# Kernel optimization log

Measured on AMD Instinct MI355X. Metric: run time of the kernel, lower is better.

## Reference

```python
import jax, jax.numpy as jnp
import numpy as np

B, S, DM, DC, L, NS = 4, 2048, 2048, 512, 4, 5  # batch, seq, d_model, d_cortical, n_layers, n_settle


def _ln(x, g, b):
    # torch nn.LayerNorm, eps=1e-5
    m = x.mean(-1, keepdims=True)
    v = ((x - m) ** 2).mean(-1, keepdims=True)
    return (x - m) * jax.lax.rsqrt(v + 1e-5) * g + b


def setup_inputs() -> dict:
    key = jax.random.key(0)
    ks = jax.random.split(key, 20)
    f = lambda k, sh: jax.random.normal(k, sh, jnp.float32) * 0.02
    return dict(
        qwen_final_hidden=jax.random.normal(ks[0], (B, S, DM), jnp.float32),
        obs=jax.random.normal(ks[1], (4, B, S, DM), jnp.float32),
        proj_W=f(ks[2], (4, DC, DM)), proj_b=f(ks[3], (4, DC)),
        fuse_W=f(ks[4], (DC, 4 * DC)), fuse_b=f(ks[5], (DC,)),
        up_W=f(ks[6], (L, DC, DC)), up_b=f(ks[7], (L, DC)),
        lateral_W=f(ks[8], (L, DC, DC)), lateral_b=f(ks[9], (L, DC)),
        precision_logit=f(ks[10], (L, DC)),
        ln_g=jnp.ones((L, DC), jnp.float32), ln_b=jnp.zeros((L, DC), jnp.float32),
        down_W=f(ks[11], (L - 1, DC, DC)), down_b=f(ks[12], (L - 1, DC)),
        out1_W=f(ks[13], (DC, DC)), out1_b=f(ks[14], (DC,)),
        out2_W=f(ks[15], (DM, DC)), out2_b=f(ks[16], (DM,)),
    )


def reference(qwen_final_hidden, obs, proj_W, proj_b, fuse_W, fuse_b,
              up_W, up_b, lateral_W, lateral_b, precision_logit,
              ln_g, ln_b, down_W, down_b, out1_W, out1_b, out2_W, out2_b):
    b, s, dm = qwen_final_hidden.shape
    # per-observed-layer input projections, concatenated along features
    proj = jnp.einsum('obsd,ocd->bsoc', obs, proj_W) + proj_b  # (B,S,4,DC)
    cat = proj.reshape(b, s, -1)
    fused = cat @ fuse_W.T + fuse_b                             # (B,S,DC)
    x0 = fused.reshape(b * s, DC)                               # per-token cortical input

    prec = jax.nn.sigmoid(precision_logit)                      # (L,DC)

    # initial bottom-up pass: activations = compress(x)
    acts = []
    x = x0
    for i in range(L):
        x = _ln(x @ up_W[i].T + up_b[i], ln_g[i], ln_b[i])
        acts.append(x)

    # settling iterations
    for _ in range(NS):
        # top-down predictions computed from pre-sweep activations
        preds = [None] * L
        for i in range(L - 1, 0, -1):
            if i < L - 1:  # top layer has no top-down weights
                preds[i - 1] = acts[i] @ down_W[i].T + down_b[i]
        x = x0
        for i in range(L):
            compressed = _ln(x @ up_W[i].T + up_b[i], ln_g[i], ln_b[i])
            target = preds[i] if preds[i] is not None else acts[i]
            werr = (compressed - target) * prec[i]
            lateral = acts[i] @ lateral_W[i].T + lateral_b[i]
            acts[i] = _ln(acts[i] + 0.5 * werr + 0.1 * lateral, ln_g[i], ln_b[i])
            x = acts[i]

    top = acts[-1]
    h = jax.nn.gelu(top @ out1_W.T + out1_b, approximate=False)
    correction = (h @ out2_W.T + out2_b).reshape(b, s, dm)
    return qwen_final_hidden + correction
```

## Files before the change

### kernel.cpp

```cpp
#include <hip/hip_runtime.h>
#include <hip/hip_bf16.h>
#include <math.h>

#define NTOK 8192
#define DMD  2048
#define DCC  512
#define TOKH 4194304

typedef __attribute__((ext_vector_type(8))) short short8;
typedef __attribute__((ext_vector_type(4))) float f32x4;

__device__ inline float bf2f(unsigned short u) {
    union { unsigned int i; float f; } x; x.i = ((unsigned int)u) << 16; return x.f;
}
__device__ inline unsigned short f2bf(float f) {
    union { float f; unsigned int i; } x; x.f = f;
    unsigned int u = x.i;
    return (unsigned short)((u + 0x7fffu + ((u >> 16) & 1u)) >> 16);
}

typedef const __attribute__((address_space(1))) unsigned int* gas1_t;
typedef __attribute__((address_space(3))) unsigned int* las3_t;
__device__ inline void async16(const void* g, void* l) {
    __builtin_amdgcn_global_load_lds(
        (gas1_t)g,
        (las3_t)(unsigned int)(unsigned long long)l, 16, 0, 0);
}

__global__ __launch_bounds__(256)
void cvt_kernel(const float* __restrict__ s, unsigned short* __restrict__ d, int n4)
{
    for (int i = blockIdx.x * 256 + threadIdx.x; i < n4; i += gridDim.x * 256) {
        float4 v = ((const float4*)s)[i];
        ushort4 o;
        o.x = f2bf(v.x); o.y = f2bf(v.y); o.z = f2bf(v.z); o.w = f2bf(v.w);
        ((ushort4*)d)[i] = o;
    }
}

struct CvtArgs { const float* src[6]; };

__global__ __launch_bounds__(256)
void wcvt_kernel(CvtArgs ca, unsigned short* __restrict__ dst)
{
    const int total = 1310720;
    for (int i = blockIdx.x * 256 + threadIdx.x; i < total; i += gridDim.x * 256) {
        const float* sp; int base;
        if      (i <  262144) { sp = ca.src[0]; base = 0;       }
        else if (i <  524288) { sp = ca.src[1]; base = 262144;  }
        else if (i <  786432) { sp = ca.src[2]; base = 524288;  }
        else if (i <  983040) { sp = ca.src[3]; base = 786432;  }
        else if (i < 1048576) { sp = ca.src[4]; base = 983040;  }
        else                  { sp = ca.src[5]; base = 1048576; }
        float4 v = ((const float4*)sp)[i - base];
        ushort4 o;
        o.x = f2bf(v.x); o.y = f2bf(v.y); o.z = f2bf(v.z); o.w = f2bf(v.w);
        ((ushort4*)dst)[i] = o;
    }
}

__global__ __launch_bounds__(256)
void ptr_kernel(const float* __restrict__ src, unsigned short* __restrict__ dst)
{
    __shared__ float t[32][33];
    const int o  = blockIdx.z;
    const int jb = blockIdx.x * 32;
    const int kb = blockIdx.y * 32;
    const int r  = threadIdx.x >> 3;
    const int c4 = (threadIdx.x & 7) * 4;
    {
        const float* s = src + ((size_t)o * DCC + kb + r) * DMD + jb + c4;
        float4 v = *(const float4*)s;
        t[r][c4+0]=v.x; t[r][c4+1]=v.y; t[r][c4+2]=v.z; t[r][c4+3]=v.w;
    }
    __syncthreads();
    {
        ushort4 u;
        u.x = f2bf(t[c4+0][r]); u.y = f2bf(t[c4+1][r]);
        u.z = f2bf(t[c4+2][r]); u.w = f2bf(t[c4+3][r]);
        *(ushort4*)(dst + ((size_t)o * DMD + jb + r) * DCC + kb + c4) = u;
    }
}

__global__ __launch_bounds__(256)
void bprime_kernel(const float* __restrict__ fuse_W, const float* __restrict__ fuse_b,
                   const float* __restrict__ proj_b, float* __restrict__ bp)
{
    const int row = blockIdx.x * 8 + (threadIdx.x >> 5);
    const int l32 = threadIdx.x & 31;
    const float* r = fuse_W + (size_t)row * (4 * DCC) + l32 * 64;
    const float* p = proj_b + l32 * 64;
    float s = 0.f;
    #pragma unroll
    for (int k = 0; k < 64; k += 4) {
        float4 v = *(const float4*)(r + k);
        float4 q = *(const float4*)(p + k);
        s += v.x*q.x + v.y*q.y + v.z*q.z + v.w*q.w;
    }
    #pragma unroll
    for (int off = 16; off; off >>= 1) s += __shfl_xor(s, off, 64);
    if (l32 == 0) bp[row] = s + fuse_b[row];
}

struct GArgs {
    const unsigned short* A[6];
    const unsigned short* W[6];
    const float*          bias[6];
    const float*          add[6];
    void*                 C[6];
};

template<bool OUTF32, bool GELU>
__global__ __launch_bounds__(256)
void gemm16(GArgs ga, int lda, int ldw, int ldadd, int ldc, int K)
{
    __shared__ unsigned short As[128 * 32];
    __shared__ unsigned short Bs[128 * 32];

    const int z    = blockIdx.z;
    const int tid  = threadIdx.x;
    const int wave = tid >> 6;
    const int lane = tid & 63;

    const int nwg   = gridDim.x * gridDim.y;
    const int bid   = blockIdx.y * gridDim.x + blockIdx.x;
    const int swz   = (bid & 7) * (nwg >> 3) + (bid >> 3);
    const int bn    = (swz % gridDim.x) * 128;
    const int bm    = (swz / gridDim.x) * 128;

    const int wr   = wave >> 1;
    const int wc   = wave & 1;

    const unsigned short* Ap = ga.A[z];
    const unsigned short* Wp = ga.W[z];

    const int lrow = lane >> 2;
    const int lcol = (lane & 3) * 8;

    f32x4 acc[4][4] = {};

    for (int k0 = 0; k0 < K; k0 += 32) {
        #pragma unroll
        for (int r = 0; r < 2; ++r) {
            int c = wave + r * 4;
            async16(Ap + (size_t)(bm + c * 16 + lrow) * lda + k0 + lcol, As + c * 512);
            async16(Wp + (size_t)(bn + c * 16 + lrow) * ldw + k0 + lcol, Bs + c * 512);
        }
        __syncthreads();

        short8 af[4], bfr[4];
        #pragma unroll
        for (int i = 0; i < 4; ++i) {
            af[i]  = *(const short8*)&As[(wr * 64 + i * 16 + (lane & 15)) * 32 + (lane >> 4) * 8];
            bfr[i] = *(const short8*)&Bs[(wc * 64 + i * 16 + (lane & 15)) * 32 + (lane >> 4) * 8];
        }
        #pragma unroll
        for (int mi = 0; mi < 4; ++mi)
            #pragma unroll
            for (int ni = 0; ni < 4; ++ni)
                acc[mi][ni] = __builtin_amdgcn_mfma_f32_16x16x32_bf16(
                    af[mi], bfr[ni], acc[mi][ni], 0, 0, 0);
        __syncthreads();
    }

    const float* bias = ga.bias[z];
    const float* add  = ga.add[z];
    #pragma unroll
    for (int ni = 0; ni < 4; ++ni) {
        int col = bn + wc * 64 + ni * 16 + (lane & 15);
        float bv = bias ? bias[col] : 0.0f;
        #pragma unroll
        for (int mi = 0; mi < 4; ++mi) {
            #pragma unroll
            for (int r = 0; r < 4; ++r) {
                int row = bm + wr * 64 + mi * 16 + (lane >> 4) * 4 + r;
                float vv = acc[mi][ni][r] + bv;
                if (GELU) vv = 0.5f * vv * (1.0f + erff(vv * 0.7071067811865475f));
                if (OUTF32) {
                    if (add) vv += add[(size_t)row * ldadd + col];
                    ((float*)ga.C[z])[(size_t)row * ldc + col] = vv;
                } else {
                    ((unsigned short*)ga.C[z])[(size_t)row * ldc + col] = f2bf(vv);
                }
            }
        }
    }
}

__global__ __launch_bounds__(256)
void x0red(const float* __restrict__ partial, const float* __restrict__ bp,
           unsigned short* __restrict__ x0)
{
    const int i = blockIdx.x * 256 + threadIdx.x;
    float4 a = ((const float4*)partial)[i];
    float4 b = ((const float4*)(partial + TOKH))[i];
    float4 c = ((const float4*)(partial + 2 * (size_t)TOKH))[i];
    float4 d = ((const float4*)(partial + 3 * (size_t)TOKH))[i];
    const int col = (i * 4) & (DCC - 1);
    float4 bv = *(const float4*)(bp + col);
    ushort4 o;
    o.x = f2bf(a.x + b.x + c.x + d.x + bv.x);
    o.y = f2bf(a.y + b.y + c.y + d.y + bv.y);
    o.z = f2bf(a.z + b.z + c.z + d.z + bv.z);
    o.w = f2bf(a.w + b.w + c.w + d.w + bv.w);
    ((ushort4*)x0)[i] = o;
}

__device__ inline int csw(int rl, int col) {
    int s = ((rl >> 2) & 3) ^ (rl & 3);
    return rl * 512 + (col ^ (s << 4));
}

template<int MODE>
__global__ __launch_bounds__(512)
void gemm_fused(const unsigned short* __restrict__ Ap,
                const unsigned short* __restrict__ Wp,
                const float* __restrict__ bias,
                const float* __restrict__ g,
                const float* __restrict__ b,
                const unsigned short* a_in,
                const unsigned short* t_in,
                const unsigned short* __restrict__ lat_in,
                const float* __restrict__ logit,
                unsigned short* outp)
{
    __shared__ unsigned short Bs[2][512 * 32];
    __shared__ unsigned short As2[2][32 * 32];
    __shared__ float red[2][8][32];

    const int tid  = threadIdx.x;
    const int wave = tid >> 6;
    const int lane = tid & 63;
    const int lrow = lane >> 2;
    const int lc8  = (lane & 3) * 8;
    const int bm   = blockIdx.x * 32;
    const int l15  = lane & 15;
    const int lh   = lane >> 4;

    f32x4 acc[2][4] = {};

    if (wave < 2)
        async16(Ap + (size_t)(bm + wave * 16 + lrow) * DCC + lc8, &As2[0][wave * 512]);
    #pragma unroll
    for (int r = 0; r < 4; ++r)
        async16(Wp + (size_t)((r * 8 + wave) * 16 + lrow) * DCC + lc8,
                &Bs[0][(r * 8 + wave) * 512]);
    __syncthreads();

    for (int t = 0; t < 16; ++t) {
        const int cur = t & 1;
        if (t < 15) {
            const int k0 = (t + 1) * 32;
            if (wave < 2)
                async16(Ap + (size_t)(bm + wave * 16 + lrow) * DCC + k0 + lc8,
                        &As2[cur ^ 1][wave * 512]);
            #pragma unroll
            for (int r = 0; r < 4; ++r)
                async16(Wp + (size_t)((r * 8 + wave) * 16 + lrow) * DCC + k0 + lc8,
                        &Bs[cur ^ 1][(r * 8 + wave) * 512]);
        }
        short8 af[2], bfr[4];
        #pragma unroll
        for (int mi = 0; mi < 2; ++mi)
            af[mi] = *(const short8*)&As2[cur][(mi * 16 + l15) * 32 + lh * 8];
        #pragma unroll
        for (int ni = 0; ni < 4; ++ni)
            bfr[ni] = *(const short8*)&Bs[cur][(wave * 64 + ni * 16 + l15) * 32 + lh * 8];
        #pragma unroll
        for (int mi = 0; mi < 2; ++mi)
            #pragma unroll
            for (int ni = 0; ni < 4; ++ni)
                acc[mi][ni] = __builtin_amdgcn_mfma_f32_16x16x32_bf16(
                    af[mi], bfr[ni], acc[mi][ni], 0, 0, 0);
        __syncthreads();
    }

    float bv[4], gv[4], bbv[4];
    #pragma unroll
    for (int ni = 0; ni < 4; ++ni) {
        int col = wave * 64 + ni * 16 + l15;
        bv[ni] = bias[col]; gv[ni] = g[col]; bbv[ni] = b[col];
    }

    float ps[2][4], pq[2][4];
    #pragma unroll
    for (int mi = 0; mi < 2; ++mi)
        #pragma unroll
        for (int rr = 0; rr < 4; ++rr) {
            float s = 0.f, q = 0.f;
            #pragma unroll
            for (int ni = 0; ni < 4; ++ni) {
                float v = acc[mi][ni][rr] + bv[ni];
                acc[mi][ni][rr] = v;
                s += v; q += v * v;
            }
            #pragma unroll
            for (int off = 1; off < 16; off <<= 1) {
                s += __shfl_xor(s, off, 64);
                q += __shfl_xor(q, off, 64);
            }
            ps[mi][rr] = s; pq[mi][rr] = q;
        }
    if (l15 == 0) {
        #pragma unroll
        for (int mi = 0; mi < 2; ++mi)
            #pragma unroll
            for (int rr = 0; rr < 4; ++rr) {
                int rl = mi * 16 + lh * 4 + rr;
                red[0][wave][rl] = ps[mi][rr];
                red[1][wave][rl] = pq[mi][rr];
            }
    }
    __syncthreads();

    unsigned short* compS = &Bs[0][0];
    #pragma unroll
    for (int mi = 0; mi < 2; ++mi)
        #pragma unroll
        for (int rr = 0; rr < 4; ++rr) {
            int rl = mi * 16 + lh * 4 + rr;
            float s = 0.f, q = 0.f;
            #pragma unroll
            for (int w = 0; w < 8; ++w) { s += red[0][w][rl]; q += red[1][w][rl]; }
            float m1 = s * (1.0f / DCC);
            float r1 = rsqrtf(q * (1.0f / DCC) - m1 * m1 + 1e-5f);
            #pragma unroll
            for (int ni = 0; ni < 4; ++ni) {
                int col = wave * 64 + ni * 16 + l15;
                compS[csw(rl, col)] = f2bf((acc[mi][ni][rr] - m1) * r1 * gv[ni] + bbv[ni]);
            }
        }
    __syncthreads();

    const int c0 = lane * 8;
    if constexpr (MODE == 0) {
        #pragma unroll
        for (int rr = 0; rr < 4; ++rr) {
            const int rl = wave * 4 + rr;
            const size_t gbase = (size_t)(bm + rl) * DCC + c0;
            short8 cm = *(const short8*)&compS[csw(rl, c0)];
            *(short8*)(outp + gbase) = cm;
        }
    } else {
        float gr[8], br[8], pr[8];
        {
            float4 g0 = *(const float4*)(g + c0),     g1 = *(const float4*)(g + c0 + 4);
            float4 b0 = *(const float4*)(b + c0),     b1 = *(const float4*)(b + c0 + 4);
            float4 p0 = *(const float4*)(logit + c0), p1 = *(const float4*)(logit + c0 + 4);
            float gt[8] = {g0.x,g0.y,g0.z,g0.w,g1.x,g1.y,g1.z,g1.w};
            float bt[8] = {b0.x,b0.y,b0.z,b0.w,b1.x,b1.y,b1.z,b1.w};
            float pt[8] = {p0.x,p0.y,p0.z,p0.w,p1.x,p1.y,p1.z,p1.w};
            #pragma unroll
            for (int j = 0; j < 8; ++j) {
                gr[j] = gt[j]; br[j] = bt[j];
                pr[j] = 1.0f / (1.0f + __expf(-pt[j]));
            }
        }
        #pragma unroll
        for (int rr = 0; rr < 4; ++rr) {
            const int rl = wave * 4 + rr;
            const size_t gbase = (size_t)(bm + rl) * DCC + c0;
            short8 cm = *(const short8*)&compS[csw(rl, c0)];
            short8 ar = *(const short8*)(a_in + gbase);
            short8 tr = *(const short8*)(t_in + gbase);
            short8 lr = *(const short8*)(lat_in + gbase);
            float tv[8], s = 0.f, q = 0.f;
            #pragma unroll
            for (int j = 0; j < 8; ++j) {
                float val = bf2f((unsigned short)ar[j])
                          + 0.5f * (bf2f((unsigned short)cm[j]) - bf2f((unsigned short)tr[j])) * pr[j]
                          + 0.1f * bf2f((unsigned short)lr[j]);
                tv[j] = val; s += val; q += val * val;
            }
            #pragma unroll
            for (int off = 1; off < 64; off <<= 1) {
                s += __shfl_xor(s, off, 64);
                q += __shfl_xor(q, off, 64);
            }
            float m2 = s * (1.0f / DCC);
            float r2 = rsqrtf(q * (1.0f / DCC) - m2 * m2 + 1e-5f);
            short8 o;
            #pragma unroll
            for (int j = 0; j < 8; ++j)
                o[j] = (short)f2bf((tv[j] - m2) * r2 * gr[j] + br[j]);
            *(short8*)(outp + gbase) = o;
        }
    }
}

extern "C" void kernel_launch(void* const* d_in, const int* in_sizes, int n_in,
                              void* d_out, int out_size, void* d_ws, size_t ws_size,
                              hipStream_t stream)
{
    const float* qwen   = (const float*)d_in[0];
    const float* obs    = (const float*)d_in[1];
    const float* proj_W = (const float*)d_in[2];
    const float* proj_b = (const float*)d_in[3];
    const float* fuse_W = (const float*)d_in[4];
    const float* fuse_b = (const float*)d_in[5];
    const float* up_W   = (const float*)d_in[6];
    const float* up_b   = (const float*)d_in[7];
    const float* lat_W  = (const float*)d_in[8];
    const float* lat_b  = (const float*)d_in[9];
    const float* plogit = (const float*)d_in[10];
    const float* ln_g   = (const float*)d_in[11];
    const float* ln_b   = (const float*)d_in[12];
    const float* down_W = (const float*)d_in[13];
    const float* down_b = (const float*)d_in[14];
    const float* out1_W = (const float*)d_in[15];
    const float* out1_b = (const float*)d_in[16];
    const float* out2_W = (const float*)d_in[17];
    const float* out2_b = (const float*)d_in[18];
    float* out = (float*)d_out;

    unsigned short* wsu = (unsigned short*)d_ws;
    float*          bp     = (float*)wsu;
    unsigned short* h16    = wsu + 2048;
    unsigned short* M16    = wsu + 8388608;
    unsigned short* x0b    = wsu + 16777216;
    unsigned short* acts16[4] = {
        wsu + 20971520, wsu + 20971520 + TOKH,
        wsu + 20971520 + 2 * TOKH, wsu + 20971520 + 3 * TOKH };
    unsigned short* w16    = wsu + 37748736;
    unsigned short* fuseW16 = w16;
    unsigned short* upW16   = w16 + 1048576;
    unsigned short* latW16  = w16 + 2097152;
    unsigned short* downW16 = w16 + 3145728;
    unsigned short* out1W16 = w16 + 3932160;
    unsigned short* out2W16 = w16 + 4194304;
    unsigned short* projT16 = wsu + 47185920;
    unsigned short* obs16   = wsu + 47185920;

    float*          part32  = (float*)d_out;
    unsigned short* outu = (unsigned short*)d_out;
    unsigned short* pred16a = outu;
    unsigned short* pred16b = outu + TOKH;
    unsigned short* lat16[4] = { outu + 2*TOKH, outu + 3*TOKH, outu + 4*TOKH, outu + 5*TOKH };

    dim3 blk(256);
    dim3 blk512(512);

    {
        CvtArgs ca;
        ca.src[0] = fuse_W; ca.src[1] = up_W;   ca.src[2] = lat_W;
        ca.src[3] = down_W; ca.src[4] = out1_W; ca.src[5] = out2_W;
        wcvt_kernel<<<dim3(2048), blk, 0, stream>>>(ca, w16);
    }
    ptr_kernel<<<dim3(DMD/32, DCC/32, 4), blk, 0, stream>>>(proj_W, projT16);
    bprime_kernel<<<dim3(DCC/8), blk, 0, stream>>>(fuse_W, fuse_b, proj_b, bp);

    {
        GArgs a{};
        for (int o = 0; o < 4; ++o) {
            a.A[o] = fuseW16 + o * DCC;
            a.W[o] = projT16 + (size_t)o * DMD * DCC;
            a.bias[o] = nullptr;
            a.C[o] = M16 + (size_t)o * DCC * DMD;
        }
        gemm16<false, false><<<dim3(DMD/128, DCC/128, 4), blk, 0, stream>>>(
            a, 4 * DCC, DCC, 0, DMD, DCC);
    }

    cvt_kernel<<<dim3(4096), blk, 0, stream>>>(obs, obs16, 16777216);

    {
        GArgs a{};
        for (int o = 0; o < 4; ++o) {
            a.A[o] = obs16 + (size_t)o * NTOK * DMD;
            a.W[o] = M16 + (size_t)o * DCC * DMD;
            a.bias[o] = nullptr;
            a.add[o]  = nullptr;
            a.C[o] = part32 + (size_t)o * TOKH;
        }
        gemm16<true, false><<<dim3(DCC/128, NTOK/128, 4), blk, 0, stream>>>(
            a, DMD, DMD, 0, DCC, DMD);
    }
    x0red<<<dim3(TOKH/4/256), blk, 0, stream>>>(part32, bp, x0b);

    dim3 fgrid(NTOK / 32);

    for (int i = 0; i < 4; ++i) {
        gemm_fused<0><<<fgrid, blk512, 0, stream>>>(
            (i == 0) ? x0b : acts16[i - 1],
            upW16 + (size_t)i * DCC * DCC, up_b + i * DCC,
            ln_g + i * DCC, ln_b + i * DCC,
            nullptr, nullptr, nullptr, nullptr, acts16[i]);
    }

    for (int s = 0; s < 5; ++s) {
        {
            GArgs a{};
            a.A[0] = acts16[1]; a.W[0] = downW16 + (size_t)1 * DCC * DCC;
            a.bias[0] = down_b + 1 * DCC; a.C[0] = pred16a;
            a.A[1] = acts16[2]; a.W[1] = downW16 + (size_t)2 * DCC * DCC;
            a.bias[1] = down_b + 2 * DCC; a.C[1] = pred16b;
            for (int i = 0; i < 4; ++i) {
                a.A[2 + i] = acts16[i];
                a.W[2 + i] = latW16 + (size_t)i * DCC * DCC;
                a.bias[2 + i] = lat_b + i * DCC;
                a.C[2 + i] = lat16[i];
            }
            gemm16<false, false><<<dim3(DCC/128, NTOK/128, 6), blk, 0, stream>>>(
                a, DCC, DCC, 0, DCC, DCC);
        }
        for (int i = 0; i < 4; ++i) {
            const unsigned short* tgt =
                (i == 0) ? pred16a : (i == 1) ? pred16b : acts16[i];
            gemm_fused<1><<<fgrid, blk512, 0, stream>>>(
                (i == 0) ? x0b : acts16[i - 1],
                upW16 + (size_t)i * DCC * DCC, up_b + i * DCC,
                ln_g + i * DCC, ln_b + i * DCC,
                acts16[i], tgt, lat16[i], plogit + i * DCC, acts16[i]);
        }
    }

    {
        GArgs a{};
        a.A[0] = acts16[3]; a.W[0] = out1W16; a.bias[0] = out1_b; a.C[0] = h16;
        gemm16<false, true><<<dim3(DCC/128, NTOK/128, 1), blk, 0, stream>>>(
            a, DCC, DCC, 0, DCC, DCC);
    }
    {
        GArgs a{};
        a.A[0] = h16; a.W[0] = out2W16; a.bias[0] = out2_b;
        a.add[0] = qwen; a.C[0] = out;
        gemm16<true, false><<<dim3(DMD/128, NTOK/128, 1), blk, 0, stream>>>(
            a, DCC, DCC, DMD, DMD, DCC);
    }
}
```

Baseline: 1.552 ms.

## Fuse all cortical layers and settling iterations into one per-token-tile megakernel

Replaces the sequence of per-layer fused GEMM launches, batched down/lateral GEMMs and the out1 GEMM with a single kernel. Each 32-token block keeps its activations in registers and shared memory across all layers and settling steps, streaming only the weights. This removes the global round-trips for activations, predictions and lateral outputs, and about 30 launches. In exchange the grid is only 256 blocks of 512 threads, so occupancy is low, weights are re-read per block, and many serialized GEMMs with syncthreads run inside one block.

```diff
diff --git a/kernel.cpp b/kernel.cpp
--- a/kernel.cpp
+++ b/kernel.cpp
@@ -6,9 +6,12 @@
 #define DMD  2048
 #define DCC  512
 #define TOKH 4194304
+#define WSZ  262144
 
 typedef __attribute__((ext_vector_type(8))) short short8;
 typedef __attribute__((ext_vector_type(4))) float f32x4;
+
+struct R4v { short8 v[4]; };
 
 __device__ inline float bf2f(unsigned short u) {
     union { unsigned int i; float f; } x; x.i = ((unsigned int)u) << 16; return x.f;
@@ -25,6 +28,11 @@
     __builtin_amdgcn_global_load_lds(
         (gas1_t)g,
         (las3_t)(unsigned int)(unsigned long long)l, 16, 0, 0);
+}
+
+__device__ inline int csw(int rl, int col) {
+    int s = ((rl >> 2) & 3) ^ (rl & 3);
+    return rl * 512 + (col ^ (s << 4));
 }
 
 __global__ __launch_bounds__(256)
@@ -206,26 +214,23 @@
     ((ushort4*)x0)[i] = o;
 }
 
-__device__ inline int csw(int rl, int col) {
-    int s = ((rl >> 2) & 3) ^ (rl & 3);
-    return rl * 512 + (col ^ (s << 4));
-}
-
-template<int MODE>
 __global__ __launch_bounds__(512)
-void gemm_fused(const unsigned short* __restrict__ Ap,
-                const unsigned short* __restrict__ Wp,
-                const float* __restrict__ bias,
-                const float* __restrict__ g,
-                const float* __restrict__ b,
-                const unsigned short* a_in,
-                const unsigned short* t_in,
-                const unsigned short* __restrict__ lat_in,
-                const float* __restrict__ logit,
-                unsigned short* outp)
-{
-    __shared__ unsigned short Bs[2][512 * 32];
-    __shared__ unsigned short As2[2][32 * 32];
+void mega_kernel(const unsigned short* __restrict__ x0b,
+                 const unsigned short* __restrict__ upW,
+                 const float* __restrict__ up_b,
+                 const unsigned short* __restrict__ latW,
+                 const float* __restrict__ lat_b,
+                 const unsigned short* __restrict__ downW,
+                 const float* __restrict__ down_b,
+                 const unsigned short* __restrict__ out1W,
+                 const float* __restrict__ out1_b,
+                 const float* __restrict__ ln_g,
+                 const float* __restrict__ ln_b,
+                 const float* __restrict__ plogit,
+                 unsigned short* __restrict__ h16)
+{
+    __shared__ unsigned short X[32 * 512];
+    __shared__ unsigned short Wb[2][512 * 32];
     __shared__ float red[2][8][32];
 
     const int tid  = threadIdx.x;
@@ -233,115 +238,147 @@
     const int lane = tid & 63;
     const int lrow = lane >> 2;
     const int lc8  = (lane & 3) * 8;
-    const int bm   = blockIdx.x * 32;
     const int l15  = lane & 15;
     const int lh   = lane >> 4;
-
-    f32x4 acc[2][4] = {};
-
-    if (wave < 2)
-        async16(Ap + (size_t)(bm + wave * 16 + lrow) * DCC + lc8, &As2[0][wave * 512]);
-    #pragma unroll
-    for (int r = 0; r < 4; ++r)
-        async16(Wp + (size_t)((r * 8 + wave) * 16 + lrow) * DCC + lc8,
-                &Bs[0][(r * 8 + wave) * 512]);
-    __syncthreads();
-
-    for (int t = 0; t < 16; ++t) {
-        const int cur = t & 1;
-        if (t < 15) {
-            const int k0 = (t + 1) * 32;
-            if (wave < 2)
-                async16(Ap + (size_t)(bm + wave * 16 + lrow) * DCC + k0 + lc8,
-                        &As2[cur ^ 1][wave * 512]);
-            #pragma unroll
-            for (int r = 0; r < 4; ++r)
-                async16(Wp + (size_t)((r * 8 + wave) * 16 + lrow) * DCC + k0 + lc8,
-                        &Bs[cur ^ 1][(r * 8 + wave) * 512]);
-        }
-        short8 af[2], bfr[4];
+    const int bm   = blockIdx.x * 32;
+    const int c0   = lane * 8;
+
+    f32x4 acc[2][4];
+
+    auto writeA = [&](R4v a) {
+        __syncthreads();
+        #pragma unroll
+        for (int rr = 0; rr < 4; ++rr)
+            *(short8*)&X[csw(wave * 4 + rr, c0)] = a.v[rr];
+        __syncthreads();
+    };
+
+    auto gemmX = [&](const unsigned short* Wp) {
         #pragma unroll
         for (int mi = 0; mi < 2; ++mi)
-            af[mi] = *(const short8*)&As2[cur][(mi * 16 + l15) * 32 + lh * 8];
-        #pragma unroll
-        for (int ni = 0; ni < 4; ++ni)
-            bfr[ni] = *(const short8*)&Bs[cur][(wave * 64 + ni * 16 + l15) * 32 + lh * 8];
+            #pragma unroll
+            for (int ni = 0; ni < 4; ++ni)
+                acc[mi][ni] = f32x4{0.f, 0.f, 0.f, 0.f};
+        #pragma unroll
+        for (int r = 0; r < 4; ++r)
+            async16(Wp + (size_t)((r * 8 + wave) * 16 + lrow) * DCC + lc8,
+                    &Wb[0][(r * 8 + wave) * 512]);
+        __syncthreads();
+        for (int t = 0; t < 16; ++t) {
+            const int cur = t & 1;
+            if (t < 15) {
+                const int k0 = (t + 1) * 32;
+                #pragma unroll
+                for (int r = 0; r < 4; ++r)
+                    async16(Wp + (size_t)((r * 8 + wave) * 16 + lrow) * DCC + k0 + lc8,
+                            &Wb[cur ^ 1][(r * 8 + wave) * 512]);
+            }
+            short8 af[2], bfr[4];
+            #pragma unroll
+            for (int mi = 0; mi < 2; ++mi)
+                af[mi] = *(const short8*)&X[csw(mi * 16 + l15, t * 32 + lh * 8)];
+            #pragma unroll
+            for (int ni = 0; ni < 4; ++ni)
+                bfr[ni] = *(const short8*)&Wb[cur][(wave * 64 + ni * 16 + l15) * 32 + lh * 8];
+            #pragma unroll
+            for (int mi = 0; mi < 2; ++mi)
+                #pragma unroll
+                for (int ni = 0; ni < 4; ++ni)
+                    acc[mi][ni] = __builtin_amdgcn_mfma_f32_16x16x32_bf16(
+                        af[mi], bfr[ni], acc[mi][ni], 0, 0, 0);
+            __syncthreads();
+        }
+    };
+
+    auto accToX = [&](const float* bias) {
+        float bv[4];
+        #pragma unroll
+        for (int ni = 0; ni < 4; ++ni) bv[ni] = bias[wave * 64 + ni * 16 + l15];
         #pragma unroll
         for (int mi = 0; mi < 2; ++mi)
             #pragma unroll
-            for (int ni = 0; ni < 4; ++ni)
-                acc[mi][ni] = __builtin_amdgcn_mfma_f32_16x16x32_bf16(
-                    af[mi], bfr[ni], acc[mi][ni], 0, 0, 0);
-        __syncthreads();
-    }
-
-    float bv[4], gv[4], bbv[4];
-    #pragma unroll
-    for (int ni = 0; ni < 4; ++ni) {
-        int col = wave * 64 + ni * 16 + l15;
-        bv[ni] = bias[col]; gv[ni] = g[col]; bbv[ni] = b[col];
-    }
-
-    float ps[2][4], pq[2][4];
-    #pragma unroll
-    for (int mi = 0; mi < 2; ++mi)
-        #pragma unroll
-        for (int rr = 0; rr < 4; ++rr) {
-            float s = 0.f, q = 0.f;
-            #pragma unroll
-            for (int ni = 0; ni < 4; ++ni) {
-                float v = acc[mi][ni][rr] + bv[ni];
-                acc[mi][ni][rr] = v;
-                s += v; q += v * v;
-            }
-            #pragma unroll
-            for (int off = 1; off < 16; off <<= 1) {
-                s += __shfl_xor(s, off, 64);
-                q += __shfl_xor(q, off, 64);
-            }
-            ps[mi][rr] = s; pq[mi][rr] = q;
-        }
-    if (l15 == 0) {
+            for (int r2 = 0; r2 < 4; ++r2) {
+                int rl = mi * 16 + lh * 4 + r2;
+                #pragma unroll
+                for (int ni = 0; ni < 4; ++ni) {
+                    int col = wave * 64 + ni * 16 + l15;
+                    X[csw(rl, col)] = f2bf(acc[mi][ni][r2] + bv[ni]);
+                }
+            }
+        __syncthreads();
+    };
+
+    auto readX = [&]() {
+        R4v r;
+        #pragma unroll
+        for (int rr = 0; rr < 4; ++rr)
+            r.v[rr] = *(const short8*)&X[csw(wave * 4 + rr, c0)];
+        return r;
+    };
+
+    auto compToX = [&](int li) {
+        const float* bias = up_b + li * DCC;
+        const float* g    = ln_g + li * DCC;
+        const float* b    = ln_b + li * DCC;
+        float bv[4], gv[4], bbv[4];
+        #pragma unroll
+        for (int ni = 0; ni < 4; ++ni) {
+            int col = wave * 64 + ni * 16 + l15;
+            bv[ni] = bias[col]; gv[ni] = g[col]; bbv[ni] = b[col];
+        }
+        float ps[2][4], pq[2][4];
         #pragma unroll
         for (int mi = 0; mi < 2; ++mi)
             #pragma unroll
-            for (int rr = 0; rr < 4; ++rr) {
-                int rl = mi * 16 + lh * 4 + rr;
-                red[0][wave][rl] = ps[mi][rr];
-                red[1][wave][rl] = pq[mi][rr];
-            }
-    }
-    __syncthreads();
-
-    unsigned short* compS = &Bs[0][0];
-    #pragma unroll
-    for (int mi = 0; mi < 2; ++mi)
-        #pragma unroll
-        for (int rr = 0; rr < 4; ++rr) {
-            int rl = mi * 16 + lh * 4 + rr;
-            float s = 0.f, q = 0.f;
-            #pragma unroll
-            for (int w = 0; w < 8; ++w) { s += red[0][w][rl]; q += red[1][w][rl]; }
-            float m1 = s * (1.0f / DCC);
-            float r1 = rsqrtf(q * (1.0f / DCC) - m1 * m1 + 1e-5f);
-            #pragma unroll
-            for (int ni = 0; ni < 4; ++ni) {
-                int col = wave * 64 + ni * 16 + l15;
-                compS[csw(rl, col)] = f2bf((acc[mi][ni][rr] - m1) * r1 * gv[ni] + bbv[ni]);
-            }
-        }
-    __syncthreads();
-
-    const int c0 = lane * 8;
-    if constexpr (MODE == 0) {
-        #pragma unroll
-        for (int rr = 0; rr < 4; ++rr) {
-            const int rl = wave * 4 + rr;
-            const size_t gbase = (size_t)(bm + rl) * DCC + c0;
-            short8 cm = *(const short8*)&compS[csw(rl, c0)];
-            *(short8*)(outp + gbase) = cm;
-        }
-    } else {
+            for (int r2 = 0; r2 < 4; ++r2) {
+                float s = 0.f, q = 0.f;
+                #pragma unroll
+                for (int ni = 0; ni < 4; ++ni) {
+                    float v = acc[mi][ni][r2] + bv[ni];
+                    acc[mi][ni][r2] = v;
+                    s += v; q += v * v;
+                }
+                #pragma unroll
+                for (int off = 1; off < 16; off <<= 1) {
+                    s += __shfl_xor(s, off, 64);
+                    q += __shfl_xor(q, off, 64);
+                }
+                ps[mi][r2] = s; pq[mi][r2] = q;
+            }
+        if (l15 == 0) {
+            #pragma unroll
+            for (int mi = 0; mi < 2; ++mi)
+                #pragma unroll
+                for (int r2 = 0; r2 < 4; ++r2) {
+                    int rl = mi * 16 + lh * 4 + r2;
+                    red[0][wave][rl] = ps[mi][r2];
+                    red[1][wave][rl] = pq[mi][r2];
+                }
+        }
+        __syncthreads();
+        #pragma unroll
+        for (int mi = 0; mi < 2; ++mi)
+            #pragma unroll
+            for (int r2 = 0; r2 < 4; ++r2) {
+                int rl = mi * 16 + lh * 4 + r2;
+                float s = 0.f, q = 0.f;
+                #pragma unroll
+                for (int w = 0; w < 8; ++w) { s += red[0][w][rl]; q += red[1][w][rl]; }
+                float m1 = s * (1.0f / DCC);
+                float r1 = rsqrtf(q * (1.0f / DCC) - m1 * m1 + 1e-5f);
+                #pragma unroll
+                for (int ni = 0; ni < 4; ++ni) {
+                    int col = wave * 64 + ni * 16 + l15;
+                    X[csw(rl, col)] = f2bf((acc[mi][ni][r2] - m1) * r1 * gv[ni] + bbv[ni]);
+                }
+            }
+        __syncthreads();
+    };
+
+    auto updateL = [&](int li, R4v aIn, R4v tgt, R4v lat) {
+        const float* g     = ln_g + li * DCC;
+        const float* b     = ln_b + li * DCC;
+        const float* logit = plogit + li * DCC;
         float gr[8], br[8], pr[8];
         {
             float4 g0 = *(const float4*)(g + c0),     g1 = *(const float4*)(g + c0 + 4);
@@ -356,20 +393,16 @@
                 pr[j] = 1.0f / (1.0f + __expf(-pt[j]));
             }
         }
+        R4v outv;
         #pragma unroll
         for (int rr = 0; rr < 4; ++rr) {
-            const int rl = wave * 4 + rr;
-            const size_t gbase = (size_t)(bm + rl) * DCC + c0;
-            short8 cm = *(const short8*)&compS[csw(rl, c0)];
-            short8 ar = *(const short8*)(a_in + gbase);
-            short8 tr = *(const short8*)(t_in + gbase);
-            short8 lr = *(const short8*)(lat_in + gbase);
+            short8 cm = *(const short8*)&X[csw(wave * 4 + rr, c0)];
             float tv[8], s = 0.f, q = 0.f;
             #pragma unroll
             for (int j = 0; j < 8; ++j) {
-                float val = bf2f((unsigned short)ar[j])
-                          + 0.5f * (bf2f((unsigned short)cm[j]) - bf2f((unsigned short)tr[j])) * pr[j]
-                          + 0.1f * bf2f((unsigned short)lr[j]);
+                float val = bf2f((unsigned short)aIn.v[rr][j])
+                          + 0.5f * (bf2f((unsigned short)cm[j]) - bf2f((unsigned short)tgt.v[rr][j])) * pr[j]
+                          + 0.1f * bf2f((unsigned short)lat.v[rr][j]);
                 tv[j] = val; s += val; q += val * val;
             }
             #pragma unroll
@@ -379,12 +412,73 @@
             }
             float m2 = s * (1.0f / DCC);
             float r2 = rsqrtf(q * (1.0f / DCC) - m2 * m2 + 1e-5f);
-            short8 o;
             #pragma unroll
             for (int j = 0; j < 8; ++j)
-                o[j] = (short)f2bf((tv[j] - m2) * r2 * gr[j] + br[j]);
-            *(short8*)(outp + gbase) = o;
-        }
+                outv.v[rr][j] = (short)f2bf((tv[j] - m2) * r2 * gr[j] + br[j]);
+        }
+        return outv;
+    };
+
+    R4v x0R;
+    #pragma unroll
+    for (int rr = 0; rr < 4; ++rr)
+        x0R.v[rr] = *(const short8*)(x0b + (size_t)(bm + wave * 4 + rr) * DCC + c0);
+
+    R4v actsR[4];
+
+    #pragma unroll
+    for (int i = 0; i < 4; ++i) {
+        writeA(i == 0 ? x0R : actsR[i - 1]);
+        gemmX(upW + (size_t)i * WSZ);
+        compToX(i);
+        actsR[i] = readX();
+    }
+
+    for (int s = 0; s < 5; ++s) {
+        writeA(actsR[1]); gemmX(downW + (size_t)1 * WSZ); accToX(down_b + DCC);
+        R4v P = readX();
+        writeA(actsR[0]); gemmX(latW); accToX(lat_b);
+        R4v Lv = readX();
+        writeA(x0R); gemmX(upW); compToX(0);
+        actsR[0] = updateL(0, actsR[0], P, Lv);
+
+        writeA(actsR[2]); gemmX(downW + (size_t)2 * WSZ); accToX(down_b + 2 * DCC);
+        P = readX();
+        writeA(actsR[1]); gemmX(latW + (size_t)1 * WSZ); accToX(lat_b + DCC);
+        Lv = readX();
+        writeA(actsR[0]); gemmX(upW + (size_t)1 * WSZ); compToX(1);
+        actsR[1] = updateL(1, actsR[1], P, Lv);
+
+        writeA(actsR[2]); gemmX(latW + (size_t)2 * WSZ); accToX(lat_b + 2 * DCC);
+        Lv = readX();
+        writeA(actsR[1]); gemmX(upW + (size_t)2 * WSZ); compToX(2);
+        actsR[2] = updateL(2, actsR[2], actsR[2], Lv);
+
+        writeA(actsR[3]); gemmX(latW + (size_t)3 * WSZ); accToX(lat_b + 3 * DCC);
+        Lv = readX();
+        writeA(actsR[2]); gemmX(upW + (size_t)3 * WSZ); compToX(3);
+        actsR[3] = updateL(3, actsR[3], actsR[3], Lv);
+    }
+
+    writeA(actsR[3]);
+    gemmX(out1W);
+    {
+        float bv[4];
+        #pragma unroll
+        for (int ni = 0; ni < 4; ++ni) bv[ni] = out1_b[wave * 64 + ni * 16 + l15];
+        #pragma unroll
+        for (int mi = 0; mi < 2; ++mi)
+            #pragma unroll
+            for (int r2 = 0; r2 < 4; ++r2) {
+                int rl = mi * 16 + lh * 4 + r2;
+                #pragma unroll
+                for (int ni = 0; ni < 4; ++ni) {
+                    int col = wave * 64 + ni * 16 + l15;
+                    float vv = acc[mi][ni][r2] + bv[ni];
+                    vv = 0.5f * vv * (1.0f + erff(vv * 0.7071067811865475f));
+                    h16[(size_t)(bm + rl) * DCC + col] = f2bf(vv);
+                }
+            }
     }
 }
 
@@ -418,9 +512,6 @@
     unsigned short* h16    = wsu + 2048;
     unsigned short* M16    = wsu + 8388608;
     unsigned short* x0b    = wsu + 16777216;
-    unsigned short* acts16[4] = {
-        wsu + 20971520, wsu + 20971520 + TOKH,
-        wsu + 20971520 + 2 * TOKH, wsu + 20971520 + 3 * TOKH };
     unsigned short* w16    = wsu + 37748736;
     unsigned short* fuseW16 = w16;
     unsigned short* upW16   = w16 + 1048576;
@@ -431,11 +522,7 @@
     unsigned short* projT16 = wsu + 47185920;
     unsigned short* obs16   = wsu + 47185920;
 
-    float*          part32  = (float*)d_out;
-    unsigned short* outu = (unsigned short*)d_out;
-    unsigned short* pred16a = outu;
-    unsigned short* pred16b = outu + TOKH;
-    unsigned short* lat16[4] = { outu + 2*TOKH, outu + 3*TOKH, outu + 4*TOKH, outu + 5*TOKH };
+    float* part32 = (float*)d_out;
 
     dim3 blk(256);
     dim3 blk512(512);
@@ -477,49 +564,10 @@
     }
     x0red<<<dim3(TOKH/4/256), blk, 0, stream>>>(part32, bp, x0b);
 
-    dim3 fgrid(NTOK / 32);
-
-    for (int i = 0; i < 4; ++i) {
-        gemm_fused<0><<<fgrid, blk512, 0, stream>>>(
-            (i == 0) ? x0b : acts16[i - 1],
-            upW16 + (size_t)i * DCC * DCC, up_b + i * DCC,
-            ln_g + i * DCC, ln_b + i * DCC,
-            nullptr, nullptr, nullptr, nullptr, acts16[i]);
-    }
-
-    for (int s = 0; s < 5; ++s) {
-        {
-            GArgs a{};
-            a.A[0] = acts16[1]; a.W[0] = downW16 + (size_t)1 * DCC * DCC;
-            a.bias[0] = down_b + 1 * DCC; a.C[0] = pred16a;
-            a.A[1] = acts16[2]; a.W[1] = downW16 + (size_t)2 * DCC * DCC;
-            a.bias[1] = down_b + 2 * DCC; a.C[1] = pred16b;
-            for (int i = 0; i < 4; ++i) {
-                a.A[2 + i] = acts16[i];
-                a.W[2 + i] = latW16 + (size_t)i * DCC * DCC;
-                a.bias[2 + i] = lat_b + i * DCC;
-                a.C[2 + i] = lat16[i];
-            }
-            gemm16<false, false><<<dim3(DCC/128, NTOK/128, 6), blk, 0, stream>>>(
-                a, DCC, DCC, 0, DCC, DCC);
-        }
-        for (int i = 0; i < 4; ++i) {
-            const unsigned short* tgt =
-                (i == 0) ? pred16a : (i == 1) ? pred16b : acts16[i];
-            gemm_fused<1><<<fgrid, blk512, 0, stream>>>(
-                (i == 0) ? x0b : acts16[i - 1],
-                upW16 + (size_t)i * DCC * DCC, up_b + i * DCC,
-                ln_g + i * DCC, ln_b + i * DCC,
-                acts16[i], tgt, lat16[i], plogit + i * DCC, acts16[i]);
-        }
-    }
-
-    {
-        GArgs a{};
-        a.A[0] = acts16[3]; a.W[0] = out1W16; a.bias[0] = out1_b; a.C[0] = h16;
-        gemm16<false, true><<<dim3(DCC/128, NTOK/128, 1), blk, 0, stream>>>(
-            a, DCC, DCC, 0, DCC, DCC);
-    }
+    mega_kernel<<<dim3(NTOK/32), blk512, 0, stream>>>(
+        x0b, upW16, up_b, latW16, lat_b, downW16, down_b,
+        out1W16, out1_b, ln_g, ln_b, plogit, h16);
+
     {
         GArgs a{};
         a.A[0] = h16; a.W[0] = out2W16; a.bias[0] = out2_b;
```

Result: slower. 3.216 ms (+107.2%).

## Fuse lateral GEMM into settle kernel and merge weight prep kernels

Applied to the files above, without the earlier changes.

The lateral projection (acts @ lateral_W) moves out of the batched gemm16 launch and into gemm_fused MODE 1. It is computed first into a new 32KB shared-memory buffer, then the up-projection runs, so the lateral result never goes to global memory as bf16 and is never read back. Separately, the three weight preprocessing kernels are combined into one launch with block-range dispatch. The change saves a full-size write and read per layer per settle step, at the cost of more LDS use per block (lower occupancy) and longer serial work inside each fused kernel.

```diff
diff --git a/kernel.cpp b/kernel.cpp
--- a/kernel.cpp
+++ b/kernel.cpp
@@ -6,6 +6,7 @@
 #define DMD  2048
 #define DCC  512
 #define TOKH 4194304
+#define WSZ  262144
 
 typedef __attribute__((ext_vector_type(8))) short short8;
 typedef __attribute__((ext_vector_type(4))) float f32x4;
@@ -25,6 +26,11 @@
     __builtin_amdgcn_global_load_lds(
         (gas1_t)g,
         (las3_t)(unsigned int)(unsigned long long)l, 16, 0, 0);
+}
+
+__device__ inline int csw(int rl, int col) {
+    int s = ((rl >> 2) & 3) ^ (rl & 3);
+    return rl * 512 + (col ^ (s << 4));
 }
 
 __global__ __launch_bounds__(256)
@@ -38,68 +44,76 @@
     }
 }
 
-struct CvtArgs { const float* src[6]; };
+struct PrepArgs {
+    const float* wsrc[6];
+    const float* proj_W;
+    const float* fuse_W;
+    const float* fuse_b;
+    const float* proj_b;
+    unsigned short* wdst;
+    unsigned short* projT;
+    float* bp;
+};
 
 __global__ __launch_bounds__(256)
-void wcvt_kernel(CvtArgs ca, unsigned short* __restrict__ dst)
-{
-    const int total = 1310720;
-    for (int i = blockIdx.x * 256 + threadIdx.x; i < total; i += gridDim.x * 256) {
-        const float* sp; int base;
-        if      (i <  262144) { sp = ca.src[0]; base = 0;       }
-        else if (i <  524288) { sp = ca.src[1]; base = 262144;  }
-        else if (i <  786432) { sp = ca.src[2]; base = 524288;  }
-        else if (i <  983040) { sp = ca.src[3]; base = 786432;  }
-        else if (i < 1048576) { sp = ca.src[4]; base = 983040;  }
-        else                  { sp = ca.src[5]; base = 1048576; }
-        float4 v = ((const float4*)sp)[i - base];
-        ushort4 o;
-        o.x = f2bf(v.x); o.y = f2bf(v.y); o.z = f2bf(v.z); o.w = f2bf(v.w);
-        ((ushort4*)dst)[i] = o;
-    }
-}
-
-__global__ __launch_bounds__(256)
-void ptr_kernel(const float* __restrict__ src, unsigned short* __restrict__ dst)
+void prep_kernel(PrepArgs pa)
 {
     __shared__ float t[32][33];
-    const int o  = blockIdx.z;
-    const int jb = blockIdx.x * 32;
-    const int kb = blockIdx.y * 32;
-    const int r  = threadIdx.x >> 3;
-    const int c4 = (threadIdx.x & 7) * 4;
-    {
-        const float* s = src + ((size_t)o * DCC + kb + r) * DMD + jb + c4;
-        float4 v = *(const float4*)s;
-        t[r][c4+0]=v.x; t[r][c4+1]=v.y; t[r][c4+2]=v.z; t[r][c4+3]=v.w;
-    }
-    __syncthreads();
-    {
-        ushort4 u;
-        u.x = f2bf(t[c4+0][r]); u.y = f2bf(t[c4+1][r]);
-        u.z = f2bf(t[c4+2][r]); u.w = f2bf(t[c4+3][r]);
-        *(ushort4*)(dst + ((size_t)o * DMD + jb + r) * DCC + kb + c4) = u;
-    }
-}
-
-__global__ __launch_bounds__(256)
-void bprime_kernel(const float* __restrict__ fuse_W, const float* __restrict__ fuse_b,
-                   const float* __restrict__ proj_b, float* __restrict__ bp)
-{
-    const int row = blockIdx.x * 8 + (threadIdx.x >> 5);
-    const int l32 = threadIdx.x & 31;
-    const float* r = fuse_W + (size_t)row * (4 * DCC) + l32 * 64;
-    const float* p = proj_b + l32 * 64;
-    float s = 0.f;
-    #pragma unroll
-    for (int k = 0; k < 64; k += 4) {
-        float4 v = *(const float4*)(r + k);
-        float4 q = *(const float4*)(p + k);
-        s += v.x*q.x + v.y*q.y + v.z*q.z + v.w*q.w;
-    }
-    #pragma unroll
-    for (int off = 16; off; off >>= 1) s += __shfl_xor(s, off, 64);
-    if (l32 == 0) bp[row] = s + fuse_b[row];
+    const int bid = blockIdx.x;
+    const int tid = threadIdx.x;
+
+    if (bid < 2048) {
+        const int total = 1310720;
+        for (int i = bid * 256 + tid; i < total; i += 2048 * 256) {
+            const float* sp; int base;
+            if      (i <  262144) { sp = pa.wsrc[0]; base = 0;       }
+            else if (i <  524288) { sp = pa.wsrc[1]; base = 262144;  }
+            else if (i <  786432) { sp = pa.wsrc[2]; base = 524288;  }
+            else if (i <  983040) { sp = pa.wsrc[3]; base = 786432;  }
+            else if (i < 1048576) { sp = pa.wsrc[4]; base = 983040;  }
+            else                  { sp = pa.wsrc[5]; base = 1048576; }
+            float4 v = ((const float4*)sp)[i - base];
+            ushort4 o;
+            o.x = f2bf(v.x); o.y = f2bf(v.y); o.z = f2bf(v.z); o.w = f2bf(v.w);
+            ((ushort4*)pa.wdst)[i] = o;
+        }
+    } else if (bid < 6144) {
+        const int b2  = bid - 2048;
+        const int o   = b2 >> 10;
+        const int rem = b2 & 1023;
+        const int jb  = (rem & 63) * 32;
+        const int kb  = (rem >> 6) * 32;
+        const int r   = tid >> 3;
+        const int c4  = (tid & 7) * 4;
+        {
+            const float* s = pa.proj_W + ((size_t)o * DCC + kb + r) * DMD + jb + c4;
+            float4 v = *(const float4*)s;
+            t[r][c4+0]=v.x; t[r][c4+1]=v.y; t[r][c4+2]=v.z; t[r][c4+3]=v.w;
+        }
+        __syncthreads();
+        {
+            ushort4 u;
+            u.x = f2bf(t[c4+0][r]); u.y = f2bf(t[c4+1][r]);
+            u.z = f2bf(t[c4+2][r]); u.w = f2bf(t[c4+3][r]);
+            *(ushort4*)(pa.projT + ((size_t)o * DMD + jb + r) * DCC + kb + c4) = u;
+        }
+    } else {
+        const int b3  = bid - 6144;
+        const int row = b3 * 8 + (tid >> 5);
+        const int l32 = tid & 31;
+        const float* r = pa.fuse_W + (size_t)row * (4 * DCC) + l32 * 64;
+        const float* p = pa.proj_b + l32 * 64;
+        float s = 0.f;
+        #pragma unroll
+        for (int k = 0; k < 64; k += 4) {
+            float4 v = *(const float4*)(r + k);
+            float4 q = *(const float4*)(p + k);
+            s += v.x*q.x + v.y*q.y + v.z*q.z + v.w*q.w;
+        }
+        #pragma unroll
+        for (int off = 16; off; off >>= 1) s += __shfl_xor(s, off, 64);
+        if (l32 == 0) pa.bp[row] = s + pa.fuse_b[row];
+    }
 }
 
 struct GArgs {
@@ -206,11 +220,6 @@
     ((ushort4*)x0)[i] = o;
 }
 
-__device__ inline int csw(int rl, int col) {
-    int s = ((rl >> 2) & 3) ^ (rl & 3);
-    return rl * 512 + (col ^ (s << 4));
-}
-
 template<int MODE>
 __global__ __launch_bounds__(512)
 void gemm_fused(const unsigned short* __restrict__ Ap,
@@ -220,12 +229,14 @@
                 const float* __restrict__ b,
                 const unsigned short* a_in,
                 const unsigned short* t_in,
-                const unsigned short* __restrict__ lat_in,
+                const unsigned short* __restrict__ latW,
+                const float* __restrict__ lat_bias,
                 const float* __restrict__ logit,
                 unsigned short* outp)
 {
     __shared__ unsigned short Bs[2][512 * 32];
     __shared__ unsigned short As2[2][32 * 32];
+    __shared__ unsigned short latS[32 * 512];
     __shared__ float red[2][8][32];
 
     const int tid  = threadIdx.x;
@@ -236,44 +247,71 @@
     const int bm   = blockIdx.x * 32;
     const int l15  = lane & 15;
     const int lh   = lane >> 4;
-
-    f32x4 acc[2][4] = {};
-
-    if (wave < 2)
-        async16(Ap + (size_t)(bm + wave * 16 + lrow) * DCC + lc8, &As2[0][wave * 512]);
-    #pragma unroll
-    for (int r = 0; r < 4; ++r)
-        async16(Wp + (size_t)((r * 8 + wave) * 16 + lrow) * DCC + lc8,
-                &Bs[0][(r * 8 + wave) * 512]);
-    __syncthreads();
-
-    for (int t = 0; t < 16; ++t) {
-        const int cur = t & 1;
-        if (t < 15) {
-            const int k0 = (t + 1) * 32;
-            if (wave < 2)
-                async16(Ap + (size_t)(bm + wave * 16 + lrow) * DCC + k0 + lc8,
-                        &As2[cur ^ 1][wave * 512]);
-            #pragma unroll
-            for (int r = 0; r < 4; ++r)
-                async16(Wp + (size_t)((r * 8 + wave) * 16 + lrow) * DCC + k0 + lc8,
-                        &Bs[cur ^ 1][(r * 8 + wave) * 512]);
-        }
-        short8 af[2], bfr[4];
+    const int c0   = lane * 8;
+
+    f32x4 acc[2][4];
+
+    auto gemmK = [&](const unsigned short* Ag, const unsigned short* Wg) {
         #pragma unroll
         for (int mi = 0; mi < 2; ++mi)
-            af[mi] = *(const short8*)&As2[cur][(mi * 16 + l15) * 32 + lh * 8];
-        #pragma unroll
-        for (int ni = 0; ni < 4; ++ni)
-            bfr[ni] = *(const short8*)&Bs[cur][(wave * 64 + ni * 16 + l15) * 32 + lh * 8];
+            #pragma unroll
+            for (int ni = 0; ni < 4; ++ni)
+                acc[mi][ni] = f32x4{0.f, 0.f, 0.f, 0.f};
+        if (wave < 2)
+            async16(Ag + (size_t)(bm + wave * 16 + lrow) * DCC + lc8, &As2[0][wave * 512]);
+        #pragma unroll
+        for (int r = 0; r < 4; ++r)
+            async16(Wg + (size_t)((r * 8 + wave) * 16 + lrow) * DCC + lc8,
+                    &Bs[0][(r * 8 + wave) * 512]);
+        __syncthreads();
+        for (int t = 0; t < 16; ++t) {
+            const int cur = t & 1;
+            if (t < 15) {
+                const int k0 = (t + 1) * 32;
+                if (wave < 2)
+                    async16(Ag + (size_t)(bm + wave * 16 + lrow) * DCC + k0 + lc8,
+                            &As2[cur ^ 1][wave * 512]);
+                #pragma unroll
+                for (int r = 0; r < 4; ++r)
+                    async16(Wg + (size_t)((r * 8 + wave) * 16 + lrow) * DCC + k0 + lc8,
+                            &Bs[cur ^ 1][(r * 8 + wave) * 512]);
+            }
+            short8 af[2], bfr[4];
+            #pragma unroll
+            for (int mi = 0; mi < 2; ++mi)
+                af[mi] = *(const short8*)&As2[cur][(mi * 16 + l15) * 32 + lh * 8];
+            #pragma unroll
+            for (int ni = 0; ni < 4; ++ni)
+                bfr[ni] = *(const short8*)&Bs[cur][(wave * 64 + ni * 16 + l15) * 32 + lh * 8];
+            #pragma unroll
+            for (int mi = 0; mi < 2; ++mi)
+                #pragma unroll
+                for (int ni = 0; ni < 4; ++ni)
+                    acc[mi][ni] = __builtin_amdgcn_mfma_f32_16x16x32_bf16(
+                        af[mi], bfr[ni], acc[mi][ni], 0, 0, 0);
+            __syncthreads();
+        }
+    };
+
+    if constexpr (MODE == 1) {
+        gemmK(a_in, latW);
+        float lb[4];
+        #pragma unroll
+        for (int ni = 0; ni < 4; ++ni) lb[ni] = lat_bias[wave * 64 + ni * 16 + l15];
         #pragma unroll
         for (int mi = 0; mi < 2; ++mi)
             #pragma unroll
-            for (int ni = 0; ni < 4; ++ni)
-                acc[mi][ni] = __builtin_amdgcn_mfma_f32_16x16x32_bf16(
-                    af[mi], bfr[ni], acc[mi][ni], 0, 0, 0);
-        __syncthreads();
-    }
+            for (int r2 = 0; r2 < 4; ++r2) {
+                int rl = mi * 16 + lh * 4 + r2;
+                #pragma unroll
+                for (int ni = 0; ni < 4; ++ni) {
+                    int col = wave * 64 + ni * 16 + l15;
+                    latS[csw(rl, col)] = f2bf(acc[mi][ni][r2] + lb[ni]);
+                }
+            }
+    }
+
+    gemmK(Ap, Wp);
 
     float bv[4], gv[4], bbv[4];
     #pragma unroll
@@ -332,7 +370,6 @@
         }
     __syncthreads();
 
-    const int c0 = lane * 8;
     if constexpr (MODE == 0) {
         #pragma unroll
         for (int rr = 0; rr < 4; ++rr) {
@@ -361,15 +398,15 @@
             const int rl = wave * 4 + rr;
             const size_t gbase = (size_t)(bm + rl) * DCC + c0;
             short8 cm = *(const short8*)&compS[csw(rl, c0)];
+            short8 lm = *(const short8*)&latS[csw(rl, c0)];
             short8 ar = *(const short8*)(a_in + gbase);
             short8 tr = *(const short8*)(t_in + gbase);
-            short8 lr = *(const short8*)(lat_in + gbase);
             float tv[8], s = 0.f, q = 0.f;
             #pragma unroll
             for (int j = 0; j < 8; ++j) {
                 float val = bf2f((unsigned short)ar[j])
                           + 0.5f * (bf2f((unsigned short)cm[j]) - bf2f((unsigned short)tr[j])) * pr[j]
-                          + 0.1f * bf2f((unsigned short)lr[j]);
+                          + 0.1f * bf2f((unsigned short)lm[j]);
                 tv[j] = val; s += val; q += val * val;
             }
             #pragma unroll
@@ -435,19 +472,19 @@
     unsigned short* outu = (unsigned short*)d_out;
     unsigned short* pred16a = outu;
     unsigned short* pred16b = outu + TOKH;
-    unsigned short* lat16[4] = { outu + 2*TOKH, outu + 3*TOKH, outu + 4*TOKH, outu + 5*TOKH };
 
     dim3 blk(256);
     dim3 blk512(512);
 
     {
-        CvtArgs ca;
-        ca.src[0] = fuse_W; ca.src[1] = up_W;   ca.src[2] = lat_W;
-        ca.src[3] = down_W; ca.src[4] = out1_W; ca.src[5] = out2_W;
-        wcvt_kernel<<<dim3(2048), blk, 0, stream>>>(ca, w16);
-    }
-    ptr_kernel<<<dim3(DMD/32, DCC/32, 4), blk, 0, stream>>>(proj_W, projT16);
-    bprime_kernel<<<dim3(DCC/8), blk, 0, stream>>>(fuse_W, fuse_b, proj_b, bp);
+        PrepArgs pa;
+        pa.wsrc[0] = fuse_W; pa.wsrc[1] = up_W;   pa.wsrc[2] = lat_W;
+        pa.wsrc[3] = down_W; pa.wsrc[4] = out1_W; pa.wsrc[5] = out2_W;
+        pa.proj_W = proj_W; pa.fuse_W = fuse_W; pa.fuse_b = fuse_b;
+        pa.proj_b = proj_b;
+        pa.wdst = w16; pa.projT = projT16; pa.bp = bp;
+        prep_kernel<<<dim3(6208), blk, 0, stream>>>(pa);
+    }
 
     {
         GArgs a{};
@@ -484,7 +521,7 @@
             (i == 0) ? x0b : acts16[i - 1],
             upW16 + (size_t)i * DCC * DCC, up_b + i * DCC,
             ln_g + i * DCC, ln_b + i * DCC,
-            nullptr, nullptr, nullptr, nullptr, acts16[i]);
+            nullptr, nullptr, nullptr, nullptr, nullptr, acts16[i]);
     }
 
     for (int s = 0; s < 5; ++s) {
@@ -494,13 +531,7 @@
             a.bias[0] = down_b + 1 * DCC; a.C[0] = pred16a;
             a.A[1] = acts16[2]; a.W[1] = downW16 + (size_t)2 * DCC * DCC;
             a.bias[1] = down_b + 2 * DCC; a.C[1] = pred16b;
-            for (int i = 0; i < 4; ++i) {
-                a.A[2 + i] = acts16[i];
-                a.W[2 + i] = latW16 + (size_t)i * DCC * DCC;
-                a.bias[2 + i] = lat_b + i * DCC;
-                a.C[2 + i] = lat16[i];
-            }
-            gemm16<false, false><<<dim3(DCC/128, NTOK/128, 6), blk, 0, stream>>>(
+            gemm16<false, false><<<dim3(DCC/128, NTOK/128, 2), blk, 0, stream>>>(
                 a, DCC, DCC, 0, DCC, DCC);
         }
         for (int i = 0; i < 4; ++i) {
@@ -510,7 +541,9 @@
                 (i == 0) ? x0b : acts16[i - 1],
                 upW16 + (size_t)i * DCC * DCC, up_b + i * DCC,
                 ln_g + i * DCC, ln_b + i * DCC,
-                acts16[i], tgt, lat16[i], plogit + i * DCC, acts16[i]);
+                acts16[i], tgt,
+                latW16 + (size_t)i * DCC * DCC, lat_b + i * DCC,
+                plogit + i * DCC, acts16[i]);
         }
     }
 
```

Result: slower. 1.707 ms (+10.0%).

## Triple-buffer fused GEMM K-loop with explicit vmcnt waits

Applied to the files above, without the earlier changes.

Changes the fused GEMM+LayerNorm kernel's K loop from double to triple buffering of A and W tiles in LDS. Two stages are prefetched ahead, and explicit s_waitcnt vmcnt counts plus raw s_barrier replace the full __syncthreads drain, so a tile's loads can stay in flight while the previous tile is computed. This raises LDS use (about 100KB for Bs), which may lower occupancy. It also depends on hand-counted vmcnt values being correct per wave.

```diff
diff --git a/kernel.cpp b/kernel.cpp
--- a/kernel.cpp
+++ b/kernel.cpp
@@ -26,6 +26,8 @@
         (gas1_t)g,
         (las3_t)(unsigned int)(unsigned long long)l, 16, 0, 0);
 }
+
+#define VMCNT(N) asm volatile("s_waitcnt vmcnt(" #N ")" ::: "memory")
 
 __global__ __launch_bounds__(256)
 void cvt_kernel(const float* __restrict__ s, unsigned short* __restrict__ d, int n4)
@@ -224,8 +226,8 @@
                 const float* __restrict__ logit,
                 unsigned short* outp)
 {
-    __shared__ unsigned short Bs[2][512 * 32];
-    __shared__ unsigned short As2[2][32 * 32];
+    __shared__ unsigned short Bs[3][512 * 32];
+    __shared__ unsigned short As3[3][32 * 32];
     __shared__ float red[2][8][32];
 
     const int tid  = threadIdx.x;
@@ -236,33 +238,35 @@
     const int bm   = blockIdx.x * 32;
     const int l15  = lane & 15;
     const int lh   = lane >> 4;
+    const int c0   = lane * 8;
 
     f32x4 acc[2][4] = {};
 
-    if (wave < 2)
-        async16(Ap + (size_t)(bm + wave * 16 + lrow) * DCC + lc8, &As2[0][wave * 512]);
-    #pragma unroll
-    for (int r = 0; r < 4; ++r)
-        async16(Wp + (size_t)((r * 8 + wave) * 16 + lrow) * DCC + lc8,
-                &Bs[0][(r * 8 + wave) * 512]);
-    __syncthreads();
-
+    auto issue = [&](int buf, int k0) {
+        if (wave < 2)
+            async16(Ap + (size_t)(bm + wave * 16 + lrow) * DCC + k0 + lc8,
+                    &As3[buf][wave * 512]);
+        #pragma unroll
+        for (int r = 0; r < 4; ++r)
+            async16(Wp + (size_t)((r * 8 + wave) * 16 + lrow) * DCC + k0 + lc8,
+                    &Bs[buf][(r * 8 + wave) * 512]);
+    };
+
+    issue(0, 0);
+    issue(1, 32);
+
+    #pragma unroll
     for (int t = 0; t < 16; ++t) {
-        const int cur = t & 1;
-        if (t < 15) {
-            const int k0 = (t + 1) * 32;
-            if (wave < 2)
-                async16(Ap + (size_t)(bm + wave * 16 + lrow) * DCC + k0 + lc8,
-                        &As2[cur ^ 1][wave * 512]);
-            #pragma unroll
-            for (int r = 0; r < 4; ++r)
-                async16(Wp + (size_t)((r * 8 + wave) * 16 + lrow) * DCC + k0 + lc8,
-                        &Bs[cur ^ 1][(r * 8 + wave) * 512]);
-        }
+        const int cur = t % 3;
+        if (t + 2 < 16) issue((t + 2) % 3, (t + 2) * 32);
+        if (t < 14)      { if (wave < 2) VMCNT(10); else VMCNT(8); }
+        else if (t == 14){ if (wave < 2) VMCNT(5);  else VMCNT(4); }
+        else             { VMCNT(0); }
+        __builtin_amdgcn_s_barrier();
         short8 af[2], bfr[4];
         #pragma unroll
         for (int mi = 0; mi < 2; ++mi)
-            af[mi] = *(const short8*)&As2[cur][(mi * 16 + l15) * 32 + lh * 8];
+            af[mi] = *(const short8*)&As3[cur][(mi * 16 + l15) * 32 + lh * 8];
         #pragma unroll
         for (int ni = 0; ni < 4; ++ni)
             bfr[ni] = *(const short8*)&Bs[cur][(wave * 64 + ni * 16 + l15) * 32 + lh * 8];
@@ -272,7 +276,7 @@
             for (int ni = 0; ni < 4; ++ni)
                 acc[mi][ni] = __builtin_amdgcn_mfma_f32_16x16x32_bf16(
                     af[mi], bfr[ni], acc[mi][ni], 0, 0, 0);
-        __syncthreads();
+        __builtin_amdgcn_s_barrier();
     }
 
     float bv[4], gv[4], bbv[4];
@@ -332,7 +336,6 @@
         }
     __syncthreads();
 
-    const int c0 = lane * 8;
     if constexpr (MODE == 0) {
         #pragma unroll
         for (int rr = 0; rr < 4; ++rr) {
```

Measured after the change: 1.484 ms. 1.05x faster.
